# Kernel optimization log

Hardware: AMD Instinct MI355X
Metric: run time of the kernel (lower is better)

The kernel has to match this reference:

```python
import jax, jax.numpy as jnp
import numpy as np

VOCAB = 50000
EMB = 128
HID = 256
H = HID // 2          # per-direction LSTM hidden
L = 59                # labelset size
B = 512
S = 256
START, STOP, PAD_LBL = 57, 58, 0
NEG = -10000.0


def setup_inputs() -> dict:
    key = jax.random.key(0)
    ks = jax.random.split(key, 12)
    inp = {}
    inp["x"] = jax.random.randint(ks[0], (B, S), 0, VOCAB)
    inp["y"] = jax.random.randint(ks[1], (B, S), 1, START)  # real labels only
    emb = jax.random.normal(ks[2], (VOCAB, EMB), jnp.float32) * 0.02
    inp["embed"] = emb.at[0].set(0.0)  # padding_idx=0

    def lstm_p(k):
        k1, k2, k3, k4 = jax.random.split(k, 4)
        s = 1.0 / np.sqrt(H)
        return (jax.random.uniform(k1, (4 * H, EMB), jnp.float32, -s, s),
                jax.random.uniform(k2, (4 * H, H), jnp.float32, -s, s),
                jax.random.uniform(k3, (4 * H,), jnp.float32, -s, s),
                jax.random.uniform(k4, (4 * H,), jnp.float32, -s, s))

    inp["Wih_f"], inp["Whh_f"], inp["bih_f"], inp["bhh_f"] = lstm_p(ks[3])
    inp["Wih_b"], inp["Whh_b"], inp["bih_b"], inp["bhh_b"] = lstm_p(ks[4])
    s = 1.0 / np.sqrt(HID)
    inp["Wout"] = jax.random.uniform(ks[5], (L, HID), jnp.float32, -s, s)
    inp["bout"] = jax.random.uniform(ks[6], (L,), jnp.float32, -s, s)
    T = jax.random.normal(ks[7], (L, L), jnp.float32)
    T = T.at[START, :].set(NEG)
    T = T.at[:, STOP].set(NEG)
    T = T.at[START, PAD_LBL].set(NEG)
    T = T.at[STOP + 1:, PAD_LBL].set(NEG)  # no-op here (STOP+1==L), kept for fidelity
    inp["trans"] = T
    inp["h0"] = jax.random.normal(ks[8], (2, B, H), jnp.float32)
    inp["c0"] = jax.random.normal(ks[9], (2, B, H), jnp.float32)
    return inp


def _lstm_scan(emb_seq, Wih, Whh, bih, bhh, h0, c0):
    # emb_seq: (S, B, E); PyTorch gate order i, f, g, o
    def step(carry, x_t):
        h, c = carry
        g = x_t @ Wih.T + bih + h @ Whh.T + bhh          # (B, 4H)
        i, f, gg, o = jnp.split(g, 4, axis=-1)
        c = jax.nn.sigmoid(f) * c + jax.nn.sigmoid(i) * jnp.tanh(gg)
        h = jax.nn.sigmoid(o) * jnp.tanh(c)
        return (h, c), h
    _, hs = jax.lax.scan(step, (h0, c0), emb_seq)
    return hs  # (S, B, H)


def reference(x, y, embed, Wih_f, Whh_f, bih_f, bhh_f,
              Wih_b, Whh_b, bih_b, bhh_b, Wout, bout, trans, h0, c0):
    # ---- BiLSTM emissions ----
    emb = embed[x]                                   # (B, S, E)
    emb = jnp.transpose(emb, (1, 0, 2))              # (S, B, E)
    hf = _lstm_scan(emb, Wih_f, Whh_f, bih_f, bhh_f, h0[0], c0[0])
    hb = _lstm_scan(emb[::-1], Wih_b, Whh_b, bih_b, bhh_b, h0[1], c0[1])[::-1]
    out = jnp.concatenate([hf, hb], axis=-1)         # (S, B, HID)
    feats = jnp.einsum('sbh,lh->bsl', out, Wout) + bout   # (B, S, L)

    # ---- CRF forward algorithm (log-sum-exp scan over time) ----
    alpha0 = jnp.full((B, L), NEG, feats.dtype).at[:, START].set(0.0)
    feats_t = jnp.transpose(feats, (1, 0, 2))        # (S, B, L)

    def fstep(alpha, f_t):
        # alpha_new[b, j] = f_t[b, j] + logsumexp_i(alpha[b, i] + trans[j, i])
        a = jax.nn.logsumexp(alpha[:, None, :] + trans[None, :, :], axis=2)
        return f_t + a, None

    alpha, _ = jax.lax.scan(fstep, alpha0, feats_t)
    fwd_score = jax.nn.logsumexp(alpha + trans[STOP][None, :], axis=1)  # (B,)

    # ---- gold path score ----
    yprev = jnp.concatenate([jnp.full((B, 1), START, y.dtype), y[:, :-1]], axis=1)
    emit = jnp.take_along_axis(feats, y[..., None], axis=2)[..., 0]     # (B, S)
    tr = trans[y, yprev]                                                # (B, S)
    gold = emit.sum(axis=1) + tr.sum(axis=1) + trans[STOP, y[:, -1]]

    return jnp.sum(fwd_score - gold)
```

## Files before the change

### kernel.cpp

```cpp
#include <hip/hip_runtime.h>

#define BB   512
#define SS   256
#define EE   128
#define HH   128
#define LL   59
#define STARTL 57
#define STOPL  58
#define VOCAB 50000

typedef float  f32x4  __attribute__((ext_vector_type(4)));
typedef short  bf16x8 __attribute__((ext_vector_type(8)));
typedef short  s16x4  __attribute__((ext_vector_type(4)));

__device__ __forceinline__ short f2bf(float f) {
    unsigned u = __float_as_uint(f);
    u += 0x7FFFu + ((u >> 16) & 1u);
    return (short)(u >> 16);
}
__device__ __forceinline__ float bf2f(unsigned short s) {
    return __uint_as_float(((unsigned)s) << 16);
}
__device__ __forceinline__ float sigf(float x) {
    float e = __builtin_amdgcn_exp2f(-1.44269504f * x);
    return __builtin_amdgcn_rcpf(1.0f + e);
}
__device__ __forceinline__ float tanhf_(float x) {
    float e = __builtin_amdgcn_exp2f(2.88539008f * x);
    return 1.0f - 2.0f * __builtin_amdgcn_rcpf(e + 1.0f);
}
__device__ __forceinline__ float wmax64(float v) {
    #pragma unroll
    for (int o = 32; o; o >>= 1) v = fmaxf(v, __shfl_xor(v, o));
    return v;
}
__device__ __forceinline__ float wsum64(float v) {
    #pragma unroll
    for (int o = 32; o; o >>= 1) v += __shfl_xor(v, o);
    return v;
}
__device__ __forceinline__ float rlane(float v, int i) {
    return __uint_as_float(__builtin_amdgcn_readlane(__float_as_uint(v), i));
}
__device__ __forceinline__ void bar_lds() {
    asm volatile("s_waitcnt lgkmcnt(0)\n\ts_barrier" ::: "memory");
}

__global__ __launch_bounds__(256) void conv_k(
    const float* __restrict__ embed,
    const float* __restrict__ Wih_f, const float* __restrict__ Wih_b,
    const float* __restrict__ Whh_f, const float* __restrict__ Whh_b,
    const float* __restrict__ bih_f, const float* __restrict__ bhh_f,
    const float* __restrict__ bih_b, const float* __restrict__ bhh_b,
    unsigned short* __restrict__ ebf, unsigned short* __restrict__ wix,
    unsigned short* __restrict__ whb, float* __restrict__ bsum)
{
    const int W1 = VOCAB * EE / 4;
    const int W2 = W1 + 2 * 16384;
    const int W3 = W2 + 2 * 16384;
    const int W4 = W3 + 1024;
    for (int i = blockIdx.x * blockDim.x + threadIdx.x; i < W4;
         i += gridDim.x * blockDim.x) {
        if (i < W1) {
            float4 v = ((const float4*)embed)[i];
            s16x4 s = { f2bf(v.x), f2bf(v.y), f2bf(v.z), f2bf(v.w) };
            ((s16x4*)ebf)[i] = s;
        } else if (i < W2) {
            const int j = i - W1, d = j >> 14, e = j & 16383;
            float4 v = ((const float4*)(d ? Wih_b : Wih_f))[e];
            s16x4 s = { f2bf(v.x), f2bf(v.y), f2bf(v.z), f2bf(v.w) };
            ((s16x4*)wix)[d * 16384 + e] = s;
        } else if (i < W3) {
            const int j = i - W2, d = j >> 14, e = j & 16383;
            float4 v = ((const float4*)(d ? Whh_b : Whh_f))[e];
            s16x4 s = { f2bf(v.x), f2bf(v.y), f2bf(v.z), f2bf(v.w) };
            ((s16x4*)whb)[d * 16384 + e] = s;
        } else {
            const int m = i - W3, d = m >> 9, c = m & 511;
            bsum[d * 512 + c] = d ? (bih_b[c] + bhh_b[c]) : (bih_f[c] + bhh_f[c]);
        }
    }
}

__global__ __launch_bounds__(512, 2) void lstm_f(
    const int* __restrict__ x, const unsigned short* __restrict__ ebf,
    const unsigned short* __restrict__ wix, const unsigned short* __restrict__ whb,
    const float* __restrict__ bsum,
    const float* __restrict__ h0, const float* __restrict__ c0,
    const float* __restrict__ Wout,
    unsigned short* __restrict__ fpF, unsigned short* __restrict__ fpB)
{
    const int tid = threadIdx.x;
    const int w = tid >> 6, l = tid & 63, qd = l >> 4, n = l & 15;
    const int rt = blockIdx.x & 127, dir = blockIdx.x >> 7;
    const int b0 = rt * 4;
    unsigned short* fp = dir ? fpB : fpF;

    __shared__ __align__(16) short hbuf[2][2048];
    __shared__ __align__(16) float gxb[2][4][2048];
    __shared__ int xsh[4 * 256];

    #pragma unroll
    for (int i = 0; i < 2; ++i) ((s16x4*)hbuf)[tid + i * 512] = (s16x4)0;
    #pragma unroll
    for (int i = 0; i < 2; ++i) {
        const int k = tid + i * 512;
        xsh[k] = x[(size_t)(b0 + (k >> 8)) * SS + (k & 255)];
    }

    if (w < 4) {
        const int s0 = 2 * w, s1 = 2 * w + 1;
        bf16x8 fh0[4][4], fh1[4][4];
        #pragma unroll
        for (int g = 0; g < 4; ++g) {
            #pragma unroll
            for (int kk = 0; kk < 4; ++kk) {
                fh0[g][kk] = *(const bf16x8*)(whb + dir * 65536
                             + (size_t)(g * 128 + 16 * s0 + n) * 128 + kk * 32 + qd * 8);
                fh1[g][kk] = *(const bf16x8*)(whb + dir * 65536
                             + (size_t)(g * 128 + 16 * s1 + n) * 128 + kk * 32 + qd * 8);
            }
        }
        bf16x8 wb[4];
        {
            const int col = w * 16 + n;
            #pragma unroll
            for (int kk = 0; kk < 4; ++kk) {
                bf16x8 v = (bf16x8)0;
                if (col < LL) {
                    const float* p = Wout + (size_t)col * 256 + dir * 128 + kk * 32 + qd * 8;
                    #pragma unroll
                    for (int j = 0; j < 8; ++j) v[j] = f2bf(p[j]);
                }
                wb[kk] = v;
            }
        }
        float cst0 = c0[((size_t)dir * BB + b0 + qd) * HH + 16 * s0 + n];
        float cst1 = c0[((size_t)dir * BB + b0 + qd) * HH + 16 * s1 + n];

        __syncthreads();
        {
            const int j = tid >> 7, c = tid & 127;
            hbuf[0][((c >> 3) * 16 + 4 * j) * 8 + (c & 7)] =
                f2bf(h0[((size_t)dir * BB + b0 + j) * HH + c]);
        }
        __syncthreads();

        const int hid0 = 16 * s0 + n, hc0 = hid0 >> 3, ho0 = hid0 & 7;
        const int hid1 = 16 * s1 + n, hc1 = hid1 >> 3, ho1 = hid1 & 7;
        const int gs0 = (s0 * 64 + qd * 16 + n) * 4;
        const int gs1 = (s1 * 64 + qd * 16 + n) * 4;

        f32x4 a0[4], a1[4], pa;
        #pragma unroll
        for (int g = 0; g < 4; ++g) {
            a0[g] = (f32x4){0.f, 0.f, 0.f, 0.f};
            a1[g] = (f32x4){0.f, 0.f, 0.f, 0.f};
        }
        pa = (f32x4){0.f, 0.f, 0.f, 0.f};

        unsigned short* fpp = fp + ((size_t)(b0 + qd) * SS + (dir ? SS - 1 : 0)) * 64
                            + w * 16 + n;
        const ptrdiff_t fpd = dir ? -64 : 64;

        for (int ts = 0; ts < SS; ++ts) {
            const int cur = ts & 1, nxt = cur ^ 1;
            const int gbuf = (ts >> 2) & 1, tau = ts & 3;

            const f32x4 g0 = *(const f32x4*)&gxb[gbuf][tau][gs0];
            const f32x4 g1 = *(const f32x4*)&gxb[gbuf][tau][gs1];

            bf16x8 ah[4];
            #pragma unroll
            for (int kk = 0; kk < 4; ++kk)
                ah[kk] = *(const bf16x8*)&hbuf[cur][((kk * 4 + qd) * 16 + n) * 8];

            a0[0][0] = g0[0]; a0[1][0] = g0[1]; a0[2][0] = g0[2]; a0[3][0] = g0[3];
            a1[0][0] = g1[0]; a1[1][0] = g1[1]; a1[2][0] = g1[2]; a1[3][0] = g1[3];

            #pragma unroll
            for (int kk = 0; kk < 4; ++kk) {
                #pragma unroll
                for (int g = 0; g < 4; ++g) {
                    a0[g] = __builtin_amdgcn_mfma_f32_16x16x32_bf16(ah[kk], fh0[g][kk], a0[g], 0, 0, 0);
                    a1[g] = __builtin_amdgcn_mfma_f32_16x16x32_bf16(ah[kk], fh1[g][kk], a1[g], 0, 0, 0);
                }
            }

            if (ts > 0) {
                pa[0] = 0.f;
                #pragma unroll
                for (int kk = 0; kk < 4; ++kk)
                    pa = __builtin_amdgcn_mfma_f32_16x16x32_bf16(ah[kk], wb[kk], pa, 0, 0, 0);
                *fpp = (unsigned short)f2bf(pa[0]);
                fpp += fpd;
            }

            {
                const float iv0 = sigf(a0[0][0]), fv0 = sigf(a0[1][0]);
                const float gv0 = tanhf_(a0[2][0]), ov0 = sigf(a0[3][0]);
                const float cc0 = fv0 * cst0 + iv0 * gv0;
                cst0 = cc0;
                hbuf[nxt][(hc0 * 16 + 4 * qd) * 8 + ho0] = f2bf(ov0 * tanhf_(cc0));
                const float iv1 = sigf(a1[0][0]), fv1 = sigf(a1[1][0]);
                const float gv1 = tanhf_(a1[2][0]), ov1 = sigf(a1[3][0]);
                const float cc1 = fv1 * cst1 + iv1 * gv1;
                cst1 = cc1;
                hbuf[nxt][(hc1 * 16 + 4 * qd) * 8 + ho1] = f2bf(ov1 * tanhf_(cc1));
            }
            bar_lds();
        }

        {
            pa[0] = 0.f;
            #pragma unroll
            for (int kk = 0; kk < 4; ++kk) {
                const bf16x8 a = *(const bf16x8*)&hbuf[0][((kk * 4 + qd) * 16 + n) * 8];
                pa = __builtin_amdgcn_mfma_f32_16x16x32_bf16(a, wb[kk], pa, 0, 0, 0);
            }
            *fpp = (unsigned short)f2bf(pa[0]);
        }
    } else {
        const int s0 = 2 * (w - 4), s1 = s0 + 1;
        bf16x8 fx0[4][4], fx1[4][4]; float bs0[4], bs1[4];
        #pragma unroll
        for (int g = 0; g < 4; ++g) {
            bs0[g] = bsum[dir * 512 + g * 128 + 16 * s0 + n];
            bs1[g] = bsum[dir * 512 + g * 128 + 16 * s1 + n];
            #pragma unroll
            for (int kk = 0; kk < 4; ++kk) {
                fx0[g][kk] = *(const bf16x8*)(wix + dir * 65536
                             + (size_t)(g * 128 + 16 * s0 + n) * 128 + kk * 32 + qd * 8);
                fx1[g][kk] = *(const bf16x8*)(wix + dir * 65536
                             + (size_t)(g * 128 + 16 * s1 + n) * 128 + kk * 32 + qd * 8);
            }
        }
        const int gs0 = (s0 * 64 + qd * 16 + n) * 4;
        const int gs1 = (s1 * 64 + qd * 16 + n) * 4;
        const int jb   = n >> 2;
        const int tau  = n & 3;
        const int jrow = jb * 256;

        auto loadfrag = [&](int G, bf16x8* e) {
            const int t  = 4 * G + tau;
            const int te = dir ? (SS - 1 - t) : t;
            const int xi = xsh[jrow + te];
            const unsigned short* er = ebf + (size_t)xi * EE + qd * 8;
            e[0] = *(const bf16x8*)(er);
            e[1] = *(const bf16x8*)(er + 32);
            e[2] = *(const bf16x8*)(er + 64);
            e[3] = *(const bf16x8*)(er + 96);
        };
        auto computeS = [&](const bf16x8* e, const bf16x8 (*fx)[4],
                            const float* bs, int gsv, int buf) {
            f32x4 c[4] = { {0,0,0,0}, {0,0,0,0}, {0,0,0,0}, {0,0,0,0} };
            #pragma unroll
            for (int g = 0; g < 4; ++g) {
                #pragma unroll
                for (int kk = 0; kk < 4; ++kk)
                    c[g] = __builtin_amdgcn_mfma_f32_16x16x32_bf16(e[kk], fx[g][kk], c[g], 0, 0, 0);
            }
            #pragma unroll
            for (int r = 0; r < 4; ++r) {
                f32x4 p = { c[0][r] + bs[0], c[1][r] + bs[1],
                            c[2][r] + bs[2], c[3][r] + bs[3] };
                *(f32x4*)&gxb[buf][r][gsv] = p;
            }
        };

        __syncthreads();
        bf16x8 eA[4], eB[4];
        loadfrag(0, eA);
        computeS(eA, fx0, bs0, gs0, 0);
        computeS(eA, fx1, bs1, gs1, 0);
        loadfrag(1, eB);
        __syncthreads();

        auto xgroup = [&](int G, bf16x8* use, bf16x8* pre) {
            if (G + 2 < SS / 4) loadfrag(G + 2, pre);
            if (G + 1 < SS / 4) computeS(use, fx0, bs0, gs0, (G + 1) & 1);
            bar_lds();
            if (G + 1 < SS / 4) computeS(use, fx1, bs1, gs1, (G + 1) & 1);
            bar_lds();
            bar_lds();
            bar_lds();
        };
        for (int G = 0; G < SS / 4; G += 2) {
            xgroup(G,     eB, eA);
            xgroup(G + 1, eA, eB);
        }
    }
}

__global__ __launch_bounds__(128, 1) void crf_k(
    const unsigned short* __restrict__ fpF, const unsigned short* __restrict__ fpB,
    const float* __restrict__ bout, const int* __restrict__ y,
    const float* __restrict__ trans, float* __restrict__ out)
{
    const int tid = threadIdx.x;
    const int wv = tid >> 6;
    const int j = tid & 63;
    const int b = blockIdx.x;
    const size_t bS = (size_t)b * SS;
    const bool valid = (j < LL);
    const int  jr = valid ? j : (LL - 1);
    const float L2E = 1.44269504f, LN2 = 0.69314718f;

    __shared__ float exch[64];
    __shared__ float gshare;

    float etr[LL];
    #pragma unroll
    for (int i = 0; i < LL; ++i) {
        const float t = wv ? trans[i * LL + jr] : trans[jr * LL + i];
        etr[i] = valid ? __builtin_amdgcn_exp2f(t * L2E) : 0.0f;
    }
    const float bo = valid ? bout[jr] : 0.0f;

    float st;
    if (wv == 0) st = valid ? ((j == STARTL) ? 0.0f : -10000.0f * L2E) : -1e30f;
    else         st = valid ? trans[STOPL * LL + jr] * L2E : -1e30f;
    float Kn = 0.0f;

    auto tAt = [&](int u) { return wv ? (SS - 1 - u) : u; };

    float fF[8], fB[8];
    #pragma unroll
    for (int q = 0; q < 8; ++q) {
        const int t = tAt(q);
        fF[q] = bf2f(fpF[(bS + t) * 64 + j]);
        fB[q] = bf2f(fpB[(bS + t) * 64 + j]);
    }

    for (int u0 = 0; u0 < SS / 2; u0 += 8) {
        float nF[8], nB[8];
        #pragma unroll
        for (int q = 0; q < 8; ++q) { nF[q] = 0.0f; nB[q] = 0.0f; }
        if (u0 + 8 < SS / 2) {
            #pragma unroll
            for (int q = 0; q < 8; ++q) {
                const int t = tAt(u0 + 8 + q);
                nF[q] = bf2f(fpF[(bS + t) * 64 + j]);
                nB[q] = bf2f(fpB[(bS + t) * 64 + j]);
            }
        }
        float fs[8];
        #pragma unroll
        for (int q = 0; q < 8; ++q) fs[q] = (fF[q] + fB[q] + bo) * L2E;

        #pragma unroll
        for (int u = 0; u < 8; ++u) {
            if (wv == 0) {
                const float Kc = Kn;
                const float ea = __builtin_amdgcn_exp2f(st - Kc);
                Kn = fmaxf(rlane(st, 1), rlane(st, STARTL));
                float d0 = 0.f, d1 = 0.f, d2 = 0.f, d3 = 0.f;
                float d4 = 0.f, d5 = 0.f, d6 = 0.f, d7 = 0.f;
                #pragma unroll
                for (int i = 0; i < 56; i += 8) {
                    d0 += etr[i]     * rlane(ea, i);
                    d1 += etr[i + 1] * rlane(ea, i + 1);
                    d2 += etr[i + 2] * rlane(ea, i + 2);
                    d3 += etr[i + 3] * rlane(ea, i + 3);
                    d4 += etr[i + 4] * rlane(ea, i + 4);
                    d5 += etr[i + 5] * rlane(ea, i + 5);
                    d6 += etr[i + 6] * rlane(ea, i + 6);
                    d7 += etr[i + 7] * rlane(ea, i + 7);
                }
                d0 += etr[56] * rlane(ea, 56);
                d1 += etr[57] * rlane(ea, 57);
                d2 += etr[58] * rlane(ea, 58);
                const float dot = ((d0 + d1) + (d2 + d3)) + ((d4 + d5) + (d6 + d7));
                st = fs[u] + Kc + __builtin_amdgcn_logf(dot);
            } else {
                const float g = fs[u] + st;
                const float Kc = Kn;
                const float eg = __builtin_amdgcn_exp2f(g - Kc);
                Kn = rlane(g, 1);
                float d0 = 0.f, d1 = 0.f, d2 = 0.f, d3 = 0.f;
                float d4 = 0.f, d5 = 0.f, d6 = 0.f, d7 = 0.f;
                #pragma unroll
                for (int i = 0; i < 56; i += 8) {
                    d0 += etr[i]     * rlane(eg, i);
                    d1 += etr[i + 1] * rlane(eg, i + 1);
                    d2 += etr[i + 2] * rlane(eg, i + 2);
                    d3 += etr[i + 3] * rlane(eg, i + 3);
                    d4 += etr[i + 4] * rlane(eg, i + 4);
                    d5 += etr[i + 5] * rlane(eg, i + 5);
                    d6 += etr[i + 6] * rlane(eg, i + 6);
                    d7 += etr[i + 7] * rlane(eg, i + 7);
                }
                d0 += etr[56] * rlane(eg, 56);
                d1 += etr[57] * rlane(eg, 57);
                d2 += etr[58] * rlane(eg, 58);
                const float dot = ((d0 + d1) + (d2 + d3)) + ((d4 + d5) + (d6 + d7));
                st = Kc + __builtin_amdgcn_logf(dot);
            }
        }
        #pragma unroll
        for (int q = 0; q < 8; ++q) { fF[q] = nF[q]; fB[q] = nB[q]; }
    }

    if (wv == 1) {
        float g = 0.0f;
        #pragma unroll
        for (int q = 0; q < 4; ++q) {
            const int t  = q * 64 + j;
            const int yt = y[bS + t];
            const int yp = t ? y[bS + t - 1] : STARTL;
            g += bf2f(fpF[(bS + t) * 64 + yt]) + bf2f(fpB[(bS + t) * 64 + yt])
               + bout[yt] + trans[yt * LL + yp];
        }
        g = wsum64(g);
        if (j == 0) {
            g += trans[STOPL * LL + y[bS + SS - 1]];
            gshare = g;
        }
        exch[j] = st;
    }
    __syncthreads();
    if (wv == 0) {
        const float v2 = valid ? (st + exch[j]) : -1e30f;
        const float m2 = wmax64(v2);
        const float s  = wsum64(__builtin_amdgcn_exp2f(v2 - m2));
        const float fwd = LN2 * (m2 + __builtin_amdgcn_logf(s));
        if (j == 0) atomicAdd(out, fwd - gshare);
    }
}

extern "C" void kernel_launch(void* const* d_in, const int* in_sizes, int n_in,
                              void* d_out, int out_size, void* d_ws, size_t ws_size,
                              hipStream_t stream)
{
    (void)in_sizes; (void)n_in; (void)out_size; (void)ws_size;
    const int*   x      = (const int*)  d_in[0];
    const int*   y      = (const int*)  d_in[1];
    const float* embed  = (const float*)d_in[2];
    const float* Wih_f  = (const float*)d_in[3];
    const float* Whh_f  = (const float*)d_in[4];
    const float* bih_f  = (const float*)d_in[5];
    const float* bhh_f  = (const float*)d_in[6];
    const float* Wih_b  = (const float*)d_in[7];
    const float* Whh_b  = (const float*)d_in[8];
    const float* bih_b  = (const float*)d_in[9];
    const float* bhh_b  = (const float*)d_in[10];
    const float* Wout   = (const float*)d_in[11];
    const float* bout   = (const float*)d_in[12];
    const float* trans  = (const float*)d_in[13];
    const float* h0     = (const float*)d_in[14];
    const float* c0     = (const float*)d_in[15];

    const size_t MiB = 1ull << 20;
    unsigned short* fpF  = (unsigned short*)d_ws;
    unsigned short* fpB  = (unsigned short*)((char*)d_ws + 16 * MiB);
    unsigned short* ebf  = (unsigned short*)((char*)d_ws + 32 * MiB);
    unsigned short* wix  = (unsigned short*)((char*)d_ws + 45 * MiB);
    unsigned short* whb  = (unsigned short*)((char*)d_ws + 45 * MiB + 256 * 1024);
    float*          bsum = (float*)((char*)d_ws + 45 * MiB + 512 * 1024);

    hipMemsetAsync(d_out, 0, sizeof(float), stream);
    conv_k<<<2048, 256, 0, stream>>>(embed, Wih_f, Wih_b, Whh_f, Whh_b,
                                     bih_f, bhh_f, bih_b, bhh_b,
                                     ebf, wix, whb, bsum);
    lstm_f<<<256, 512, 0, stream>>>(x, ebf, wix, whb, bsum, h0, c0, Wout,
                                    fpF, fpB);
    crf_k<<<BB, 128, 0, stream>>>(fpF, fpB, bout, y, trans, (float*)d_out);
}
```

Before: 342.8 us.

## Fuse bf16 weight/embedding conversion into LSTM kernel; CRF dot via LDS broadcast

Drops the separate conversion kernel that turned the whole 50000x128 embedding table and the LSTM weights to bf16. The LSTM kernel now reads fp32 weights and only the embedding rows it needs, converting them in registers, and sums the two biases inline. The per-step embedding prefetch moves twice the bytes, with the conversion done after the load. In the CRF kernel the 59-wide dot product now gets its values by writing exp values to LDS and reading them back as vectors, replacing 59 readlane operations; this adds LDS traffic and relies on wave-level ordering with no explicit barrier.

```diff
diff --git a/kernel.cpp b/kernel.cpp
--- a/kernel.cpp
+++ b/kernel.cpp
@@ -46,46 +46,12 @@
     asm volatile("s_waitcnt lgkmcnt(0)\n\ts_barrier" ::: "memory");
 }
 
-__global__ __launch_bounds__(256) void conv_k(
-    const float* __restrict__ embed,
-    const float* __restrict__ Wih_f, const float* __restrict__ Wih_b,
-    const float* __restrict__ Whh_f, const float* __restrict__ Whh_b,
+__global__ __launch_bounds__(512, 2) void lstm_f(
+    const int* __restrict__ x, const float* __restrict__ embed,
+    const float* __restrict__ Wih_f, const float* __restrict__ Whh_f,
     const float* __restrict__ bih_f, const float* __restrict__ bhh_f,
+    const float* __restrict__ Wih_b, const float* __restrict__ Whh_b,
     const float* __restrict__ bih_b, const float* __restrict__ bhh_b,
-    unsigned short* __restrict__ ebf, unsigned short* __restrict__ wix,
-    unsigned short* __restrict__ whb, float* __restrict__ bsum)
-{
-    const int W1 = VOCAB * EE / 4;
-    const int W2 = W1 + 2 * 16384;
-    const int W3 = W2 + 2 * 16384;
-    const int W4 = W3 + 1024;
-    for (int i = blockIdx.x * blockDim.x + threadIdx.x; i < W4;
-         i += gridDim.x * blockDim.x) {
-        if (i < W1) {
-            float4 v = ((const float4*)embed)[i];
-            s16x4 s = { f2bf(v.x), f2bf(v.y), f2bf(v.z), f2bf(v.w) };
-            ((s16x4*)ebf)[i] = s;
-        } else if (i < W2) {
-            const int j = i - W1, d = j >> 14, e = j & 16383;
-            float4 v = ((const float4*)(d ? Wih_b : Wih_f))[e];
-            s16x4 s = { f2bf(v.x), f2bf(v.y), f2bf(v.z), f2bf(v.w) };
-            ((s16x4*)wix)[d * 16384 + e] = s;
-        } else if (i < W3) {
-            const int j = i - W2, d = j >> 14, e = j & 16383;
-            float4 v = ((const float4*)(d ? Whh_b : Whh_f))[e];
-            s16x4 s = { f2bf(v.x), f2bf(v.y), f2bf(v.z), f2bf(v.w) };
-            ((s16x4*)whb)[d * 16384 + e] = s;
-        } else {
-            const int m = i - W3, d = m >> 9, c = m & 511;
-            bsum[d * 512 + c] = d ? (bih_b[c] + bhh_b[c]) : (bih_f[c] + bhh_f[c]);
-        }
-    }
-}
-
-__global__ __launch_bounds__(512, 2) void lstm_f(
-    const int* __restrict__ x, const unsigned short* __restrict__ ebf,
-    const unsigned short* __restrict__ wix, const unsigned short* __restrict__ whb,
-    const float* __restrict__ bsum,
     const float* __restrict__ h0, const float* __restrict__ c0,
     const float* __restrict__ Wout,
     unsigned short* __restrict__ fpF, unsigned short* __restrict__ fpB)
@@ -96,6 +62,11 @@
     const int b0 = rt * 4;
     unsigned short* fp = dir ? fpB : fpF;
 
+    const float* Whh = dir ? Whh_b : Whh_f;
+    const float* Wih = dir ? Wih_b : Wih_f;
+    const float* bi  = dir ? bih_b : bih_f;
+    const float* bh  = dir ? bhh_b : bhh_f;
+
     __shared__ __align__(16) short hbuf[2][2048];
     __shared__ __align__(16) float gxb[2][4][2048];
     __shared__ int xsh[4 * 256];
@@ -108,6 +79,14 @@
         xsh[k] = x[(size_t)(b0 + (k >> 8)) * SS + (k & 255)];
     }
 
+    auto ldfrag = [&](const float* p) {
+        const float4 lo = *(const float4*)p, hi = *(const float4*)(p + 4);
+        bf16x8 v;
+        v[0] = f2bf(lo.x); v[1] = f2bf(lo.y); v[2] = f2bf(lo.z); v[3] = f2bf(lo.w);
+        v[4] = f2bf(hi.x); v[5] = f2bf(hi.y); v[6] = f2bf(hi.z); v[7] = f2bf(hi.w);
+        return v;
+    };
+
     if (w < 4) {
         const int s0 = 2 * w, s1 = 2 * w + 1;
         bf16x8 fh0[4][4], fh1[4][4];
@@ -115,10 +94,8 @@
         for (int g = 0; g < 4; ++g) {
             #pragma unroll
             for (int kk = 0; kk < 4; ++kk) {
-                fh0[g][kk] = *(const bf16x8*)(whb + dir * 65536
-                             + (size_t)(g * 128 + 16 * s0 + n) * 128 + kk * 32 + qd * 8);
-                fh1[g][kk] = *(const bf16x8*)(whb + dir * 65536
-                             + (size_t)(g * 128 + 16 * s1 + n) * 128 + kk * 32 + qd * 8);
+                fh0[g][kk] = ldfrag(Whh + (size_t)(g * 128 + 16 * s0 + n) * 128 + kk * 32 + qd * 8);
+                fh1[g][kk] = ldfrag(Whh + (size_t)(g * 128 + 16 * s1 + n) * 128 + kk * 32 + qd * 8);
             }
         }
         bf16x8 wb[4];
@@ -225,14 +202,12 @@
         bf16x8 fx0[4][4], fx1[4][4]; float bs0[4], bs1[4];
         #pragma unroll
         for (int g = 0; g < 4; ++g) {
-            bs0[g] = bsum[dir * 512 + g * 128 + 16 * s0 + n];
-            bs1[g] = bsum[dir * 512 + g * 128 + 16 * s1 + n];
-            #pragma unroll
-            for (int kk = 0; kk < 4; ++kk) {
-                fx0[g][kk] = *(const bf16x8*)(wix + dir * 65536
-                             + (size_t)(g * 128 + 16 * s0 + n) * 128 + kk * 32 + qd * 8);
-                fx1[g][kk] = *(const bf16x8*)(wix + dir * 65536
-                             + (size_t)(g * 128 + 16 * s1 + n) * 128 + kk * 32 + qd * 8);
+            bs0[g] = bi[g * 128 + 16 * s0 + n] + bh[g * 128 + 16 * s0 + n];
+            bs1[g] = bi[g * 128 + 16 * s1 + n] + bh[g * 128 + 16 * s1 + n];
+            #pragma unroll
+            for (int kk = 0; kk < 4; ++kk) {
+                fx0[g][kk] = ldfrag(Wih + (size_t)(g * 128 + 16 * s0 + n) * 128 + kk * 32 + qd * 8);
+                fx1[g][kk] = ldfrag(Wih + (size_t)(g * 128 + 16 * s1 + n) * 128 + kk * 32 + qd * 8);
             }
         }
         const int gs0 = (s0 * 64 + qd * 16 + n) * 4;
@@ -241,15 +216,26 @@
         const int tau  = n & 3;
         const int jrow = jb * 256;
 
-        auto loadfrag = [&](int G, bf16x8* e) {
+        auto loadfrag = [&](int G, f32x4* ef) {
             const int t  = 4 * G + tau;
             const int te = dir ? (SS - 1 - t) : t;
             const int xi = xsh[jrow + te];
-            const unsigned short* er = ebf + (size_t)xi * EE + qd * 8;
-            e[0] = *(const bf16x8*)(er);
-            e[1] = *(const bf16x8*)(er + 32);
-            e[2] = *(const bf16x8*)(er + 64);
-            e[3] = *(const bf16x8*)(er + 96);
+            const float* er = embed + (size_t)xi * EE + qd * 8;
+            #pragma unroll
+            for (int kk = 0; kk < 4; ++kk) {
+                ef[kk * 2]     = *(const f32x4*)(er + kk * 32);
+                ef[kk * 2 + 1] = *(const f32x4*)(er + kk * 32 + 4);
+            }
+        };
+        auto cvt = [&](const f32x4* ef, bf16x8* e) {
+            #pragma unroll
+            for (int kk = 0; kk < 4; ++kk) {
+                const f32x4 lo = ef[kk * 2], hi = ef[kk * 2 + 1];
+                bf16x8 v;
+                v[0] = f2bf(lo[0]); v[1] = f2bf(lo[1]); v[2] = f2bf(lo[2]); v[3] = f2bf(lo[3]);
+                v[4] = f2bf(hi[0]); v[5] = f2bf(hi[1]); v[6] = f2bf(hi[2]); v[7] = f2bf(hi[3]);
+                e[kk] = v;
+            }
         };
         auto computeS = [&](const bf16x8* e, const bf16x8 (*fx)[4],
                             const float* bs, int gsv, int buf) {
@@ -269,18 +255,22 @@
         };
 
         __syncthreads();
-        bf16x8 eA[4], eB[4];
+        f32x4 eA[8], eB[8];
         loadfrag(0, eA);
-        computeS(eA, fx0, bs0, gs0, 0);
-        computeS(eA, fx1, bs1, gs1, 0);
+        {
+            bf16x8 e0[4]; cvt(eA, e0);
+            computeS(e0, fx0, bs0, gs0, 0);
+            computeS(e0, fx1, bs1, gs1, 0);
+        }
         loadfrag(1, eB);
         __syncthreads();
 
-        auto xgroup = [&](int G, bf16x8* use, bf16x8* pre) {
+        auto xgroup = [&](int G, f32x4* use, f32x4* pre) {
             if (G + 2 < SS / 4) loadfrag(G + 2, pre);
-            if (G + 1 < SS / 4) computeS(use, fx0, bs0, gs0, (G + 1) & 1);
+            bf16x8 e[4];
+            if (G + 1 < SS / 4) { cvt(use, e); computeS(e, fx0, bs0, gs0, (G + 1) & 1); }
             bar_lds();
-            if (G + 1 < SS / 4) computeS(use, fx1, bs1, gs1, (G + 1) & 1);
+            if (G + 1 < SS / 4) computeS(e, fx1, bs1, gs1, (G + 1) & 1);
             bar_lds();
             bar_lds();
             bar_lds();
@@ -306,6 +296,7 @@
     const int  jr = valid ? j : (LL - 1);
     const float L2E = 1.44269504f, LN2 = 0.69314718f;
 
+    __shared__ __align__(16) float eash[2][64];
     __shared__ float exch[64];
     __shared__ float gshare;
 
@@ -321,6 +312,32 @@
     if (wv == 0) st = valid ? ((j == STARTL) ? 0.0f : -10000.0f * L2E) : -1e30f;
     else         st = valid ? trans[STOPL * LL + jr] * L2E : -1e30f;
     float Kn = 0.0f;
+
+    float* myea = &eash[wv][0];
+
+    auto lsedot = [&](float ex) {
+        myea[j] = ex;
+        f32x4 e4[15];
+        #pragma unroll
+        for (int q = 0; q < 15; ++q) e4[q] = *(const f32x4*)(myea + 4 * q);
+        float d0 = 0.f, d1 = 0.f, d2 = 0.f, d3 = 0.f;
+        float d4 = 0.f, d5 = 0.f, d6 = 0.f, d7 = 0.f;
+        #pragma unroll
+        for (int i = 0; i < 56; i += 8) {
+            d0 += etr[i]     * e4[(i    ) >> 2][(i    ) & 3];
+            d1 += etr[i + 1] * e4[(i + 1) >> 2][(i + 1) & 3];
+            d2 += etr[i + 2] * e4[(i + 2) >> 2][(i + 2) & 3];
+            d3 += etr[i + 3] * e4[(i + 3) >> 2][(i + 3) & 3];
+            d4 += etr[i + 4] * e4[(i + 4) >> 2][(i + 4) & 3];
+            d5 += etr[i + 5] * e4[(i + 5) >> 2][(i + 5) & 3];
+            d6 += etr[i + 6] * e4[(i + 6) >> 2][(i + 6) & 3];
+            d7 += etr[i + 7] * e4[(i + 7) >> 2][(i + 7) & 3];
+        }
+        d0 += etr[56] * e4[14][0];
+        d1 += etr[57] * e4[14][1];
+        d2 += etr[58] * e4[14][2];
+        return ((d0 + d1) + (d2 + d3)) + ((d4 + d5) + (d6 + d7));
+    };
 
     auto tAt = [&](int u) { return wv ? (SS - 1 - u) : u; };
 
@@ -354,46 +371,14 @@
                 const float Kc = Kn;
                 const float ea = __builtin_amdgcn_exp2f(st - Kc);
                 Kn = fmaxf(rlane(st, 1), rlane(st, STARTL));
-                float d0 = 0.f, d1 = 0.f, d2 = 0.f, d3 = 0.f;
-                float d4 = 0.f, d5 = 0.f, d6 = 0.f, d7 = 0.f;
-                #pragma unroll
-                for (int i = 0; i < 56; i += 8) {
-                    d0 += etr[i]     * rlane(ea, i);
-                    d1 += etr[i + 1] * rlane(ea, i + 1);
-                    d2 += etr[i + 2] * rlane(ea, i + 2);
-                    d3 += etr[i + 3] * rlane(ea, i + 3);
-                    d4 += etr[i + 4] * rlane(ea, i + 4);
-                    d5 += etr[i + 5] * rlane(ea, i + 5);
-                    d6 += etr[i + 6] * rlane(ea, i + 6);
-                    d7 += etr[i + 7] * rlane(ea, i + 7);
-                }
-                d0 += etr[56] * rlane(ea, 56);
-                d1 += etr[57] * rlane(ea, 57);
-                d2 += etr[58] * rlane(ea, 58);
-                const float dot = ((d0 + d1) + (d2 + d3)) + ((d4 + d5) + (d6 + d7));
+                const float dot = lsedot(ea);
                 st = fs[u] + Kc + __builtin_amdgcn_logf(dot);
             } else {
                 const float g = fs[u] + st;
                 const float Kc = Kn;
                 const float eg = __builtin_amdgcn_exp2f(g - Kc);
                 Kn = rlane(g, 1);
-                float d0 = 0.f, d1 = 0.f, d2 = 0.f, d3 = 0.f;
-                float d4 = 0.f, d5 = 0.f, d6 = 0.f, d7 = 0.f;
-                #pragma unroll
-                for (int i = 0; i < 56; i += 8) {
-                    d0 += etr[i]     * rlane(eg, i);
-                    d1 += etr[i + 1] * rlane(eg, i + 1);
-                    d2 += etr[i + 2] * rlane(eg, i + 2);
-                    d3 += etr[i + 3] * rlane(eg, i + 3);
-                    d4 += etr[i + 4] * rlane(eg, i + 4);
-                    d5 += etr[i + 5] * rlane(eg, i + 5);
-                    d6 += etr[i + 6] * rlane(eg, i + 6);
-                    d7 += etr[i + 7] * rlane(eg, i + 7);
-                }
-                d0 += etr[56] * rlane(eg, 56);
-                d1 += etr[57] * rlane(eg, 57);
-                d2 += etr[58] * rlane(eg, 58);
-                const float dot = ((d0 + d1) + (d2 + d3)) + ((d4 + d5) + (d6 + d7));
+                const float dot = lsedot(eg);
                 st = Kc + __builtin_amdgcn_logf(dot);
             }
         }
@@ -451,18 +436,13 @@
     const float* c0     = (const float*)d_in[15];
 
     const size_t MiB = 1ull << 20;
-    unsigned short* fpF  = (unsigned short*)d_ws;
-    unsigned short* fpB  = (unsigned short*)((char*)d_ws + 16 * MiB);
-    unsigned short* ebf  = (unsigned short*)((char*)d_ws + 32 * MiB);
-    unsigned short* wix  = (unsigned short*)((char*)d_ws + 45 * MiB);
-    unsigned short* whb  = (unsigned short*)((char*)d_ws + 45 * MiB + 256 * 1024);
-    float*          bsum = (float*)((char*)d_ws + 45 * MiB + 512 * 1024);
+    unsigned short* fpF = (unsigned short*)d_ws;
+    unsigned short* fpB = (unsigned short*)((char*)d_ws + 16 * MiB);
 
     hipMemsetAsync(d_out, 0, sizeof(float), stream);
-    conv_k<<<2048, 256, 0, stream>>>(embed, Wih_f, Wih_b, Whh_f, Whh_b,
-                                     bih_f, bhh_f, bih_b, bhh_b,
-                                     ebf, wix, whb, bsum);
-    lstm_f<<<256, 512, 0, stream>>>(x, ebf, wix, whb, bsum, h0, c0, Wout,
-                                    fpF, fpB);
+    lstm_f<<<256, 512, 0, stream>>>(x, embed,
+                                    Wih_f, Whh_f, bih_f, bhh_f,
+                                    Wih_b, Whh_b, bih_b, bhh_b,
+                                    h0, c0, Wout, fpF, fpB);
     crf_k<<<BB, 128, 0, stream>>>(fpF, fpB, bout, y, trans, (float*)d_out);
 }
```

Measured after the change: 411.5 us. 1.2x slower.
